# Performance work log

Hardware: AMD Instinct MI355X
Metric: run time of the kernel (lower is better)

## Reference

```python
import jax, jax.numpy as jnp
import numpy as np


def setup_inputs() -> dict:
    key = jax.random.key(0)
    k1, k2, k3, k4 = jax.random.split(key, 4)
    B, T, N, D = 4, 8, 512, 256
    BT = B * T
    x = jax.random.normal(k1, (BT, N, D), dtype=jnp.float32)
    A_causal = jax.random.uniform(k2, (B, N, N), dtype=jnp.float32)
    W_qkv = jax.random.normal(k3, (3 * D, D), dtype=jnp.float32) * (D ** -0.5)
    W_proj = jax.random.normal(k4, (D, D), dtype=jnp.float32) * (D ** -0.5)
    b_proj = jnp.zeros((D,), dtype=jnp.float32)
    causal_lambda = jnp.ones((1,), dtype=jnp.float32) * 0.1
    return {
        "x": x,
        "A_causal": A_causal,
        "W_qkv": W_qkv,
        "W_proj": W_proj,
        "b_proj": b_proj,
        "causal_lambda": causal_lambda,
        "num_frames": 8,
    }


def reference(x, A_causal, W_qkv, W_proj, b_proj, causal_lambda, num_frames):
    BT, N, D = x.shape
    H = 8
    hd = D // H
    scale = hd ** -0.5
    # qkv projection (torch Linear: x @ W.T), split into q,k,v of shape [BT,H,N,hd]
    qkv = (x @ W_qkv.T).reshape(BT, N, 3, H, hd)
    qkv = jnp.transpose(qkv, (2, 0, 3, 1, 4))  # [3,BT,H,N,hd]
    q, k, v = qkv[0], qkv[1], qkv[2]
    attn = jnp.einsum("bhnd,bhmd->bhnm", q, k) * scale  # [BT,H,N,N]
    # expand A_causal [B,N,N] over frames (axis 0) and heads (broadcast axis 1)
    A_exp = jnp.repeat(A_causal, num_frames, axis=0)[:, None, :, :]  # [BT,1,N,N]
    attn = attn + causal_lambda[0] * A_exp
    attn = jax.nn.softmax(attn, axis=-1)
    out = jnp.einsum("bhnm,bhmd->bhnd", attn, v)  # [BT,H,N,hd]
    out = jnp.transpose(out, (0, 2, 1, 3)).reshape(BT, N, D)
    return out @ W_proj.T + b_proj
```

## Files before the change

### kernel.cpp

```cpp
#include <hip/hip_runtime.h>
#include <hip/hip_bf16.h>

typedef unsigned short u16;
typedef unsigned int   u32;
typedef __attribute__((ext_vector_type(8))) short short8;
typedef __attribute__((ext_vector_type(4))) float f32x4;

static __device__ __forceinline__ u16 f2b(float f) {
    __hip_bfloat16 h = __float2bfloat16(f);
    return *reinterpret_cast<u16*>(&h);
}
static __device__ __forceinline__ u32 pk2(float a, float b) {
    return (u32)f2b(a) | ((u32)f2b(b) << 16);
}

#define LDK 72

__global__ __launch_bounds__(256) void prep(const float* __restrict__ A,
                                            const float* __restrict__ LAM,
                                            const float* __restrict__ Wq,
                                            const float* __restrict__ Wp,
                                            u16* __restrict__ AB,
                                            u16* __restrict__ wqb,
                                            u16* __restrict__ wpb) {
    const int bid = blockIdx.x;
    const float* src;
    u16* dst;
    float scale;
    int base;
    if (bid < 512)      { src = A;  dst = AB;  scale = LAM[0]; base = bid * 2048; }
    else if (bid < 608) { src = Wq; dst = wqb; scale = 1.0f;   base = (bid - 512) * 2048; }
    else                { src = Wp; dst = wpb; scale = 1.0f;   base = (bid - 608) * 2048; }
    const int i = base + threadIdx.x * 8;
    const float4 a = *(const float4*)(src + i);
    const float4 b = *(const float4*)(src + i + 4);
    uint4 o;
    o.x = pk2(scale * a.x, scale * a.y);
    o.y = pk2(scale * a.z, scale * a.w);
    o.z = pk2(scale * b.x, scale * b.y);
    o.w = pk2(scale * b.z, scale * b.w);
    *(uint4*)(dst + i) = o;
}

__global__ __launch_bounds__(256) void qkv_gemm(const float* __restrict__ X,
                                                const u16* __restrict__ WB,
                                                u16* __restrict__ qo,
                                                u16* __restrict__ ko,
                                                u16* __restrict__ vt) {
    __shared__ u16 SH[2 * 128 * LDK];
    u16* Xs = SH;
    u16* Ws = SH + 128 * LDK;
    const int t    = threadIdx.x;
    const int m0   = blockIdx.x << 7;
    const int o0   = blockIdx.y << 7;
    const int lane = t & 63;
    const int wid  = t >> 6;
    const int wr   = (wid >> 1) << 6;
    const int wc   = (wid & 1) << 6;
    const int ln   = lane & 15;
    const int quad = lane >> 4;

    const int r  = t >> 1;
    const int hf = (t & 1) << 5;
    const float* xg = X + (size_t)(m0 + r) * 256 + hf;
    const u16*   wg = WB + (size_t)(o0 + r) * 256 + hf;
    uint4* xls = (uint4*)&Xs[r * LDK + hf];
    uint4* wls = (uint4*)&Ws[r * LDK + hf];

    f32x4 acc[4][4] = {};

    for (int kc = 0; kc < 256; kc += 64) {
        const float4* xp = (const float4*)(xg + kc);
        const uint4*  wp = (const uint4*)(wg + kc);
        float xv[32];
#pragma unroll
        for (int i = 0; i < 8; ++i) {
            float4 a = xp[i]; xv[4*i] = a.x; xv[4*i+1] = a.y; xv[4*i+2] = a.z; xv[4*i+3] = a.w;
        }
        uint4 w0 = wp[0], w1 = wp[1], w2 = wp[2], w3 = wp[3];
        uint4 xq[4];
#pragma unroll
        for (int i = 0; i < 4; ++i) {
            xq[i].x = pk2(xv[8*i],   xv[8*i+1]); xq[i].y = pk2(xv[8*i+2], xv[8*i+3]);
            xq[i].z = pk2(xv[8*i+4], xv[8*i+5]); xq[i].w = pk2(xv[8*i+6], xv[8*i+7]);
        }
        __syncthreads();
#pragma unroll
        for (int i = 0; i < 4; ++i) xls[i] = xq[i];
        wls[0] = w0; wls[1] = w1; wls[2] = w2; wls[3] = w3;
        __syncthreads();
#pragma unroll
        for (int kk = 0; kk < 64; kk += 32) {
            short8 a[4], b[4];
#pragma unroll
            for (int i = 0; i < 4; ++i)
                a[i] = *(const short8*)&Xs[(wr + i * 16 + ln) * LDK + kk + quad * 8];
#pragma unroll
            for (int j = 0; j < 4; ++j)
                b[j] = *(const short8*)&Ws[(wc + j * 16 + ln) * LDK + kk + quad * 8];
#pragma unroll
            for (int i = 0; i < 4; ++i)
#pragma unroll
                for (int j = 0; j < 4; ++j)
                    acc[i][j] = __builtin_amdgcn_mfma_f32_16x16x32_bf16(a[i], b[j], acc[i][j], 0, 0, 0);
        }
    }

    const int which = o0 >> 8;
    if (which < 2) {
        const float qscale = (which == 0) ? 0.17677669529663689f : 1.0f;
        u16* dst = (which == 0) ? qo : ko;
#pragma unroll
        for (int i = 0; i < 4; ++i) {
            const int mb = m0 + wr + i * 16 + quad * 4;
#pragma unroll
            for (int j = 0; j < 4; ++j) {
                const int o   = o0 + wc + j * 16 + ln;
                const int rem = o & 255;
                const int hh  = rem >> 5;
                const int dd  = rem & 31;
#pragma unroll
                for (int rr = 0; rr < 4; ++rr) {
                    const int m  = mb + rr;
                    const int bt = m >> 9;
                    const int n  = m & 511;
                    dst[(((size_t)bt * 8 + hh) * 512 + n) * 32 + dd] = f2b(acc[i][j][rr] * qscale);
                }
            }
        }
    } else {
        __syncthreads();
        u16* T = SH;
#pragma unroll
        for (int i = 0; i < 4; ++i) {
            const int ml = wr + i * 16 + quad * 4;
#pragma unroll
            for (int j = 0; j < 4; ++j) {
                const int ol = wc + j * 16 + ln;
                uint2 pv;
                pv.x = pk2(acc[i][j][0], acc[i][j][1]);
                pv.y = pk2(acc[i][j][2], acc[i][j][3]);
                *(uint2*)&T[ol * 136 + ml] = pv;
            }
        }
        __syncthreads();
        const int row = t >> 1;
        const int seg = (t & 1) << 6;
        const int o   = o0 + row;
        const int rem = o & 255;
        const int hh  = rem >> 5;
        const int dd  = rem & 31;
        const int bt  = m0 >> 9;
        u16* dstv = vt + (((size_t)bt * 8 + hh) * 32 + dd) * 512 + (m0 & 511) + seg;
#pragma unroll
        for (int kk2 = 0; kk2 < 8; ++kk2) {
            uint4 val = *(const uint4*)&T[row * 136 + seg + kk2 * 8];
            *(uint4*)(dstv + kk2 * 8) = val;
        }
    }
}

__global__ __launch_bounds__(256, 4) void attn_mfma(const u16* __restrict__ Q,
                                                    const u16* __restrict__ K,
                                                    const u16* __restrict__ VT,
                                                    const u16* __restrict__ AB,
                                                    const int* __restrict__ NF,
                                                    u16* __restrict__ AO) {
    __shared__ u16 Ks[2][64 * 40];
    __shared__ u16 Vs[2][32 * 72];
    __shared__ u16 Ps[4][32 * 40];
    const int t    = threadIdx.x;
    const int w    = t >> 6;
    const int lane = t & 63;
    const int ln   = lane & 15;
    const int quad = lane >> 4;
    const int L    = blockIdx.x;
    const int g    = (L & 7) + (((L >> 3) & 1) << 3);
    const int j    = L >> 4;
    const int qt   = g & 3;
    const int h    = j & 7;
    const int bt   = (g >> 2) * 8 + (j >> 3);
    const int bh   = bt * 8 + h;
    const int q0   = qt * 128 + w * 32;
    const size_t base = (size_t)bh * (512 * 32);
    const int b    = bt / NF[0];
    const u16* Ab  = AB + (size_t)b * 512 * 512;
    const u16* Ar0 = Ab + (size_t)(q0 + ln) * 512 + quad * 4;
    const u16* Ar1 = Ab + (size_t)(q0 + 16 + ln) * 512 + quad * 4;

    const int krow = t >> 2, kcol = (t & 3) * 8;
    const int vd   = t >> 3, vn   = (t & 7) * 8;
    const u16* Kg = K + base;
    const u16* Vg = VT + base;

    {
        uint4 s0 = *(const uint4*)(Kg + (size_t)krow * 32 + kcol);
        uint4 s2 = *(const uint4*)(Vg + (size_t)vd * 512 + vn);
        *(uint4*)&Ks[0][krow * 40 + kcol] = s0;
        *(uint4*)&Vs[0][vd * 72 + vn]     = s2;
    }
    uint2 ar[8];
#pragma unroll
    for (int mt = 0; mt < 4; ++mt) {
        ar[2*mt]     = *(const uint2*)(Ar0 + mt * 16);
        ar[2*mt + 1] = *(const uint2*)(Ar1 + mt * 16);
    }

    short8 qf[2];
#pragma unroll
    for (int nt = 0; nt < 2; ++nt)
        qf[nt] = *(const short8*)(Q + base + (size_t)(q0 + nt * 16 + ln) * 32 + quad * 8);

    f32x4 o[2][2] = {};
    float lsum0 = 0.f, lsum1 = 0.f;
    __syncthreads();

    int cur = 0;
    for (int jt = 0; jt < 512; jt += 64) {
        const int nxt = cur ^ 1;
        const int jn  = (jt + 64) & 511;
        uint4 t0 = *(const uint4*)(Kg + (size_t)(jn + krow) * 32 + kcol);
        uint4 t2 = *(const uint4*)(Vg + (size_t)vd * 512 + jn + vn);
        uint2 arn[8];
#pragma unroll
        for (int mt = 0; mt < 4; ++mt) {
            arn[2*mt]     = *(const uint2*)(Ar0 + jn + mt * 16);
            arn[2*mt + 1] = *(const uint2*)(Ar1 + jn + mt * 16);
        }

        float ps0 = 0.f, ps1 = 0.f;
#pragma unroll
        for (int ks = 0; ks < 2; ++ks) {
#pragma unroll
            for (int mm = 0; mm < 2; ++mm) {
                const int mt = 2 * ks + mm;
                short8 ka = *(const short8*)&Ks[cur][(mt * 16 + ln) * 40 + quad * 8];
                f32x4 c0, c1;
                c0[0] = __uint_as_float(ar[2*mt].x << 16);   c0[1] = __uint_as_float(ar[2*mt].x & 0xffff0000u);
                c0[2] = __uint_as_float(ar[2*mt].y << 16);   c0[3] = __uint_as_float(ar[2*mt].y & 0xffff0000u);
                c1[0] = __uint_as_float(ar[2*mt+1].x << 16); c1[1] = __uint_as_float(ar[2*mt+1].x & 0xffff0000u);
                c1[2] = __uint_as_float(ar[2*mt+1].y << 16); c1[3] = __uint_as_float(ar[2*mt+1].y & 0xffff0000u);
                const f32x4 s0 = __builtin_amdgcn_mfma_f32_16x16x32_bf16(ka, qf[0], c0, 0, 0, 0);
                const f32x4 s1 = __builtin_amdgcn_mfma_f32_16x16x32_bf16(ka, qf[1], c1, 0, 0, 0);
                const float p00 = __expf(s0[0]), p01 = __expf(s0[1]), p02 = __expf(s0[2]), p03 = __expf(s0[3]);
                const float p10 = __expf(s1[0]), p11 = __expf(s1[1]), p12 = __expf(s1[2]), p13 = __expf(s1[3]);
                ps0 += (p00 + p01) + (p02 + p03);
                ps1 += (p10 + p11) + (p12 + p13);
                uint2 w0; w0.x = pk2(p00, p01); w0.y = pk2(p02, p03);
                uint2 w1; w1.x = pk2(p10, p11); w1.y = pk2(p12, p13);
                *(uint2*)&Ps[w][ln * 40 + mm * 16 + quad * 4]        = w0;
                *(uint2*)&Ps[w][(16 + ln) * 40 + mm * 16 + quad * 4] = w1;
            }
            short8 pa0 = *(const short8*)&Ps[w][ln * 40 + quad * 8];
            short8 pa1 = *(const short8*)&Ps[w][(16 + ln) * 40 + quad * 8];
            short8 vb0 = *(const short8*)&Vs[cur][ln * 72 + ks * 32 + quad * 8];
            short8 vb1 = *(const short8*)&Vs[cur][(16 + ln) * 72 + ks * 32 + quad * 8];
            o[0][0] = __builtin_amdgcn_mfma_f32_16x16x32_bf16(pa0, vb0, o[0][0], 0, 0, 0);
            o[0][1] = __builtin_amdgcn_mfma_f32_16x16x32_bf16(pa0, vb1, o[0][1], 0, 0, 0);
            o[1][0] = __builtin_amdgcn_mfma_f32_16x16x32_bf16(pa1, vb0, o[1][0], 0, 0, 0);
            o[1][1] = __builtin_amdgcn_mfma_f32_16x16x32_bf16(pa1, vb1, o[1][1], 0, 0, 0);
        }

        *(uint4*)&Ks[nxt][krow * 40 + kcol] = t0;
        *(uint4*)&Vs[nxt][vd * 72 + vn]     = t2;
        ps0 += __shfl_xor(ps0, 16); ps0 += __shfl_xor(ps0, 32); lsum0 += ps0;
        ps1 += __shfl_xor(ps1, 16); ps1 += __shfl_xor(ps1, 32); lsum1 += ps1;
        __syncthreads();
#pragma unroll
        for (int i = 0; i < 8; ++i) ar[i] = arn[i];
        cur = nxt;
    }

#pragma unroll
    for (int r = 0; r < 4; ++r) {
        const int src = quad * 4 + r;
        const float i0 = 1.f / __shfl(lsum0, src);
        const float i1 = 1.f / __shfl(lsum1, src);
        const int n0 = qt * 128 + w * 32 + quad * 4 + r;
#pragma unroll
        for (int ntd = 0; ntd < 2; ++ntd) {
            AO[((size_t)bt * 512 + n0) * 256 + h * 32 + ntd * 16 + ln]      = f2b(o[0][ntd][r] * i0);
            AO[((size_t)bt * 512 + n0 + 16) * 256 + h * 32 + ntd * 16 + ln] = f2b(o[1][ntd][r] * i1);
        }
    }
}

__global__ __launch_bounds__(256) void proj_gemm(const u16* __restrict__ X,
                                                 const u16* __restrict__ WB,
                                                 const float* __restrict__ BIAS,
                                                 float* __restrict__ OUT) {
    __shared__ u16 Xs[128 * LDK];
    __shared__ u16 Ws[128 * LDK];
    const int t    = threadIdx.x;
    const int m0   = blockIdx.x << 7;
    const int o0   = blockIdx.y << 7;
    const int lane = t & 63;
    const int wid  = t >> 6;
    const int wr   = (wid >> 1) << 6;
    const int wc   = (wid & 1) << 6;
    const int ln   = lane & 15;
    const int quad = lane >> 4;

    const int r  = t >> 1;
    const int hf = (t & 1) << 5;
    const u16* xg = X + (size_t)(m0 + r) * 256 + hf;
    const u16* wg = WB + (size_t)(o0 + r) * 256 + hf;
    uint4* xls = (uint4*)&Xs[r * LDK + hf];
    uint4* wls = (uint4*)&Ws[r * LDK + hf];

    f32x4 acc[4][4] = {};

    for (int kc = 0; kc < 256; kc += 64) {
        const uint4* xp = (const uint4*)(xg + kc);
        const uint4* wp = (const uint4*)(wg + kc);
        uint4 x0 = xp[0], x1 = xp[1], x2 = xp[2], x3 = xp[3];
        uint4 w0 = wp[0], w1 = wp[1], w2 = wp[2], w3 = wp[3];
        __syncthreads();
        xls[0] = x0; xls[1] = x1; xls[2] = x2; xls[3] = x3;
        wls[0] = w0; wls[1] = w1; wls[2] = w2; wls[3] = w3;
        __syncthreads();
#pragma unroll
        for (int kk = 0; kk < 64; kk += 32) {
            short8 a[4], b[4];
#pragma unroll
            for (int i = 0; i < 4; ++i)
                a[i] = *(const short8*)&Xs[(wr + i * 16 + ln) * LDK + kk + quad * 8];
#pragma unroll
            for (int j = 0; j < 4; ++j)
                b[j] = *(const short8*)&Ws[(wc + j * 16 + ln) * LDK + kk + quad * 8];
#pragma unroll
            for (int i = 0; i < 4; ++i)
#pragma unroll
                for (int j = 0; j < 4; ++j)
                    acc[i][j] = __builtin_amdgcn_mfma_f32_16x16x32_bf16(a[i], b[j], acc[i][j], 0, 0, 0);
        }
    }

#pragma unroll
    for (int i = 0; i < 4; ++i) {
        const int mb = m0 + wr + i * 16 + quad * 4;
#pragma unroll
        for (int j = 0; j < 4; ++j) {
            const int o  = o0 + wc + j * 16 + ln;
            const float bo = BIAS[o];
#pragma unroll
            for (int rr = 0; rr < 4; ++rr) {
                const int m = mb + rr;
                OUT[(size_t)m * 256 + o] = acc[i][j][rr] + bo;
            }
        }
    }
}

extern "C" void kernel_launch(void* const* d_in, const int* in_sizes, int n_in,
                              void* d_out, int out_size, void* d_ws, size_t ws_size,
                              hipStream_t stream) {
    (void)in_sizes; (void)n_in; (void)out_size; (void)ws_size;
    const float* x     = (const float*)d_in[0];
    const float* A     = (const float*)d_in[1];
    const float* Wqkv  = (const float*)d_in[2];
    const float* Wproj = (const float*)d_in[3];
    const float* bproj = (const float*)d_in[4];
    const float* lam   = (const float*)d_in[5];
    const int*   nf    = (const int*)d_in[6];
    float* out = (float*)d_out;

    u16* q   = (u16*)d_ws;
    u16* k   = q + 4194304;
    u16* vt  = k + 4194304;
    u16* ao  = vt + 4194304;
    u16* AB  = ao + 4194304;
    u16* wqb = AB + 1048576;
    u16* wpb = wqb + 196608;

    prep    <<<dim3(640), 256, 0, stream>>>(A, lam, Wqkv, Wproj, AB, wqb, wpb);
    qkv_gemm<<<dim3(128, 6), 256, 0, stream>>>(x, wqb, q, k, vt);
    attn_mfma<<<dim3(1024), 256, 0, stream>>>(q, k, vt, AB, nf, ao);
    proj_gemm<<<dim3(128, 2), 256, 0, stream>>>(ao, wpb, bproj, out);
}
```

Measured before the change: 154.1 us.

## Pre-convert x to bf16 in prep kernel and remap attention block order

Measured after the change: 144.4 us. 6.3% less time.

```diff
diff --git a/kernel.cpp b/kernel.cpp
--- a/kernel.cpp
+++ b/kernel.cpp
@@ -16,10 +16,12 @@
 
 #define LDK 72
 
-__global__ __launch_bounds__(256) void prep(const float* __restrict__ A,
+__global__ __launch_bounds__(256) void prep(const float* __restrict__ X,
+                                            const float* __restrict__ A,
                                             const float* __restrict__ LAM,
                                             const float* __restrict__ Wq,
                                             const float* __restrict__ Wp,
+                                            u16* __restrict__ xb,
                                             u16* __restrict__ AB,
                                             u16* __restrict__ wqb,
                                             u16* __restrict__ wpb) {
@@ -28,9 +30,10 @@
     u16* dst;
     float scale;
     int base;
-    if (bid < 512)      { src = A;  dst = AB;  scale = LAM[0]; base = bid * 2048; }
-    else if (bid < 608) { src = Wq; dst = wqb; scale = 1.0f;   base = (bid - 512) * 2048; }
-    else                { src = Wp; dst = wpb; scale = 1.0f;   base = (bid - 608) * 2048; }
+    if (bid < 2048)      { src = X;  dst = xb;  scale = 1.0f;   base = bid * 2048; }
+    else if (bid < 2560) { src = A;  dst = AB;  scale = LAM[0]; base = (bid - 2048) * 2048; }
+    else if (bid < 2656) { src = Wq; dst = wqb; scale = 1.0f;   base = (bid - 2560) * 2048; }
+    else                 { src = Wp; dst = wpb; scale = 1.0f;   base = (bid - 2656) * 2048; }
     const int i = base + threadIdx.x * 8;
     const float4 a = *(const float4*)(src + i);
     const float4 b = *(const float4*)(src + i + 4);
@@ -42,7 +45,7 @@
     *(uint4*)(dst + i) = o;
 }
 
-__global__ __launch_bounds__(256) void qkv_gemm(const float* __restrict__ X,
+__global__ __launch_bounds__(256) void qkv_gemm(const u16* __restrict__ XB,
                                                 const u16* __restrict__ WB,
                                                 u16* __restrict__ qo,
                                                 u16* __restrict__ ko,
@@ -62,31 +65,20 @@
 
     const int r  = t >> 1;
     const int hf = (t & 1) << 5;
-    const float* xg = X + (size_t)(m0 + r) * 256 + hf;
-    const u16*   wg = WB + (size_t)(o0 + r) * 256 + hf;
+    const u16* xg = XB + (size_t)(m0 + r) * 256 + hf;
+    const u16* wg = WB + (size_t)(o0 + r) * 256 + hf;
     uint4* xls = (uint4*)&Xs[r * LDK + hf];
     uint4* wls = (uint4*)&Ws[r * LDK + hf];
 
     f32x4 acc[4][4] = {};
 
     for (int kc = 0; kc < 256; kc += 64) {
-        const float4* xp = (const float4*)(xg + kc);
-        const uint4*  wp = (const uint4*)(wg + kc);
-        float xv[32];
-#pragma unroll
-        for (int i = 0; i < 8; ++i) {
-            float4 a = xp[i]; xv[4*i] = a.x; xv[4*i+1] = a.y; xv[4*i+2] = a.z; xv[4*i+3] = a.w;
-        }
+        const uint4* xp = (const uint4*)(xg + kc);
+        const uint4* wp = (const uint4*)(wg + kc);
+        uint4 x0 = xp[0], x1 = xp[1], x2 = xp[2], x3 = xp[3];
         uint4 w0 = wp[0], w1 = wp[1], w2 = wp[2], w3 = wp[3];
-        uint4 xq[4];
-#pragma unroll
-        for (int i = 0; i < 4; ++i) {
-            xq[i].x = pk2(xv[8*i],   xv[8*i+1]); xq[i].y = pk2(xv[8*i+2], xv[8*i+3]);
-            xq[i].z = pk2(xv[8*i+4], xv[8*i+5]); xq[i].w = pk2(xv[8*i+6], xv[8*i+7]);
-        }
-        __syncthreads();
-#pragma unroll
-        for (int i = 0; i < 4; ++i) xls[i] = xq[i];
+        __syncthreads();
+        xls[0] = x0; xls[1] = x1; xls[2] = x2; xls[3] = x3;
         wls[0] = w0; wls[1] = w1; wls[2] = w2; wls[3] = w3;
         __syncthreads();
 #pragma unroll
@@ -175,11 +167,10 @@
     const int ln   = lane & 15;
     const int quad = lane >> 4;
     const int L    = blockIdx.x;
-    const int g    = (L & 7) + (((L >> 3) & 1) << 3);
-    const int j    = L >> 4;
-    const int qt   = g & 3;
-    const int h    = j & 7;
-    const int bt   = (g >> 2) * 8 + (j >> 3);
+    const int rr_  = L >> 3;
+    const int qt   = rr_ & 3;
+    const int h    = (rr_ >> 2) & 7;
+    const int bt   = (L & 7) * 4 + (rr_ >> 5);
     const int bh   = bt * 8 + h;
     const int q0   = qt * 128 + w * 32;
     const size_t base = (size_t)bh * (512 * 32);
@@ -369,12 +360,13 @@
     u16* k   = q + 4194304;
     u16* vt  = k + 4194304;
     u16* ao  = vt + 4194304;
-    u16* AB  = ao + 4194304;
+    u16* xb  = ao + 4194304;
+    u16* AB  = xb + 4194304;
     u16* wqb = AB + 1048576;
     u16* wpb = wqb + 196608;
 
-    prep    <<<dim3(640), 256, 0, stream>>>(A, lam, Wqkv, Wproj, AB, wqb, wpb);
-    qkv_gemm<<<dim3(128, 6), 256, 0, stream>>>(x, wqb, q, k, vt);
+    prep     <<<dim3(2688), 256, 0, stream>>>(x, A, lam, Wqkv, Wproj, xb, AB, wqb, wpb);
+    qkv_gemm <<<dim3(128, 6), 256, 0, stream>>>(xb, wqb, q, k, vt);
     attn_mfma<<<dim3(1024), 256, 0, stream>>>(q, k, vt, AB, nf, ao);
     proj_gemm<<<dim3(128, 2), 256, 0, stream>>>(ao, wpb, bproj, out);
 }
```
